# Kernel optimization log

Measured on AMD Instinct MI355X. Metric: run time of the kernel, lower is better.

The kernel has to match this reference:

```python
import jax, jax.numpy as jnp
import numpy as np

BS, N, D, B, D_PM = 8, 4096, 1024, 8, 64
BUDGET = 16.0


def setup_inputs() -> dict:
    key = jax.random.key(0)
    ks = jax.random.split(key, 6)
    H = jax.random.normal(ks[0], (BS, N, D), jnp.float32)
    surprise = jax.random.normal(ks[1], (BS, N, D), jnp.float32)
    # W_pm initialized as (1/B)*I + small noise, as in initialize()
    eye = jnp.eye(D_PM, dtype=jnp.float32)
    W_pm = eye / B + 0.01 * jax.random.normal(ks[2], (BS, B, D_PM, D_PM), jnp.float32)
    proj_in_w = jax.random.normal(ks[3], (D_PM, D), jnp.float32) / np.float32(np.sqrt(D))
    proj_in_b = jnp.zeros((D_PM,), jnp.float32)
    # original zero-inits proj_out; use small values so output is non-trivial
    proj_out_w = 0.02 * jax.random.normal(ks[4], (D, D_PM), jnp.float32)
    proj_out_b = jnp.zeros((D,), jnp.float32)
    raw_beta = jnp.full((B,), -3.0, jnp.float32)
    raw_decay = jnp.full((B,), np.float32(np.log(0.999 / 0.001)), jnp.float32)  # logit(0.999)
    surp_scale = jnp.ones((1,), jnp.float32)
    surp_bias = jnp.zeros((1,), jnp.float32)
    return dict(H=H, surprise=surprise, W_pm=W_pm,
                proj_in_w=proj_in_w, proj_in_b=proj_in_b,
                proj_out_w=proj_out_w, proj_out_b=proj_out_b,
                raw_beta=raw_beta, raw_decay=raw_decay,
                surp_scale=surp_scale, surp_bias=surp_bias)


def reference(H, surprise, W_pm, proj_in_w, proj_in_b, proj_out_w, proj_out_b,
              raw_beta, raw_decay, surp_scale, surp_bias):
    # ---- read ----
    pre = jnp.einsum('bnd,pd->bnp', H, proj_in_w) + proj_in_b          # [BS,N,D_pm]
    W_sum = jnp.sum(W_pm, axis=1)                                      # [BS,D_pm,D_pm]
    post = jnp.einsum('bnp,bqp->bnq', pre, W_sum)                      # pre @ W_sum^T
    pm_read = jnp.einsum('bnq,dq->bnd', post, proj_out_w) + proj_out_b # [BS,N,D]
    # ---- commit (Hebbian, surprise-gated) ----
    surp_mag = jnp.linalg.norm(surprise, axis=-1)                      # [BS,N]
    s = jax.nn.sigmoid(surp_scale * surp_mag + surp_bias)              # [BS,N]
    weighted = jnp.sqrt(s)[..., None] * pre                            # [BS,N,D_pm]
    G = jnp.einsum('bnp,bnq->bpq', weighted, weighted) / N             # [BS,D_pm,D_pm]
    beta = jax.nn.softplus(raw_beta)                                   # [B]
    decay = jax.nn.sigmoid(raw_decay)                                  # [B]
    eye = jnp.eye(D_PM, dtype=pre.dtype)
    T = decay[None, :, None, None] * eye + beta[None, :, None, None] * G[:, None]  # [BS,B,D_pm,D_pm]
    W_new = jnp.einsum('bkij,bkjq->bkiq', W_pm, T)                     # [BS,B,D_pm,D_pm]
    frob = jnp.sqrt(jnp.sum(W_new * W_new, axis=(-2, -1), keepdims=True))
    scale = jnp.minimum(BUDGET / jnp.maximum(frob, 1e-8), 1.0)
    W_new = W_new * scale
    return pm_read, W_new
```

## Files before the change

kernel.cpp:

```cpp
#include <hip/hip_runtime.h>

typedef unsigned short u16;
typedef __attribute__((ext_vector_type(4))) float f32x4;
typedef __attribute__((ext_vector_type(8))) short s16x8;

static constexpr int N_ = 4096;
static constexpr int D_ = 1024;

__device__ __forceinline__ u16 f2bf(float f) {
  unsigned u = __float_as_uint(f);
  u += 0x7FFFu + ((u >> 16) & 1u);
  return (u16)(u >> 16);
}

__device__ __forceinline__ f32x4 zero4() {
  f32x4 z; z[0] = 0.f; z[1] = 0.f; z[2] = 0.f; z[3] = 0.f; return z;
}

__global__ __launch_bounds__(256) void k_prep(
    const float* __restrict__ Wpm, const float* __restrict__ piw,
    const float* __restrict__ pw, u16* __restrict__ WpB,
    u16* __restrict__ MB) {
  int bid = blockIdx.x, tid = threadIdx.x;
  if (bid < 16) {
    size_t i0 = (size_t)bid * 4096;
    for (int idx = tid; idx < 4096; idx += 256)
      WpB[i0 + idx] = f2bf(piw[i0 + idx]);
    return;
  }
  __shared__ float Ws[64][65];
  int idx2 = bid - 16;
  int b = idx2 >> 4, t = idx2 & 15;
  for (int idx = tid; idx < 4096; idx += 256) {
    float s = 0.f;
#pragma unroll
    for (int k = 0; k < 8; ++k)
      s += Wpm[((size_t)(b * 8 + k)) * 4096 + idx];
    Ws[idx >> 6][idx & 63] = s;
  }
  __syncthreads();
  u16* mb = MB + ((size_t)b << 16);
  for (int oidx = tid; oidx < 4096; oidx += 256) {
    int r = oidx >> 6, c = oidx & 63;
    int drow = t * 64 + r;
    const float* prow = pw + (size_t)drow * 64;
    float acc = 0.f;
#pragma unroll 8
    for (int q = 0; q < 64; ++q) acc += prow[q] * Ws[q][c];
    mb[(size_t)drow * 64 + c] = f2bf(acc);
  }
}

__global__ __launch_bounds__(512, 4) void k_main(
    const float* __restrict__ H, const float* __restrict__ Sur,
    const float* __restrict__ pib, const float* __restrict__ pob,
    const float* __restrict__ sscale_p, const float* __restrict__ sbias_p,
    const u16* __restrict__ WpB, const u16* __restrict__ MB,
    float* __restrict__ Gacc, float* __restrict__ out) {
  __shared__ float preF[64][68];
  __shared__ u16 preRP[64][72];
  __shared__ u16 wRP[64][72];
  __shared__ float sqs[64];

  const int tid = threadIdx.x;
  const int lane = tid & 63;
  const int w = tid >> 6;
  const int wm = w & 3;
  const int wk = w >> 2;
  const int llo = lane & 15;
  const int lhi = lane >> 4;
  const int b = blockIdx.x >> 6;
  const int row0 = (blockIdx.x & 63) * 64;

  {
    int r = w * 8 + (lane >> 3);
    const float* p = Sur + ((size_t)b * N_ + row0 + r) * D_ + (lane & 7) * 4;
    float a0 = 0.f, a1 = 0.f;
#pragma unroll 8
    for (int j = 0; j < 32; j += 2) {
      float4 v = *(const float4*)(p + j * 32);
      float4 v2 = *(const float4*)(p + j * 32 + 32);
      a0 += v.x * v.x + v.y * v.y + v.z * v.z + v.w * v.w;
      a1 += v2.x * v2.x + v2.y * v2.y + v2.z * v2.z + v2.w * v2.w;
    }
    float a = a0 + a1;
    a += __shfl_xor(a, 1, 64);
    a += __shfl_xor(a, 2, 64);
    a += __shfl_xor(a, 4, 64);
    if ((lane & 7) == 0) {
      float mag = sqrtf(a);
      float s = 1.f / (1.f + __expf(-(sscale_p[0] * mag + sbias_p[0])));
      sqs[r] = sqrtf(s);
    }
  }

  f32x4 accA[4];
#pragma unroll
  for (int t = 0; t < 4; ++t) accA[t] = zero4();
  {
    const float* hrow =
        H + ((size_t)b * N_ + row0 + wm * 16 + llo) * D_ + wk * 512 + lhi * 8;
    const u16* wp0 = WpB + (size_t)llo * 1024 + wk * 512 + lhi * 8;
#pragma unroll 2
    for (int k0 = 0; k0 < 512; k0 += 32) {
      float4 a0 = *(const float4*)(hrow + k0);
      float4 a1 = *(const float4*)(hrow + k0 + 4);
      s16x8 af;
      af[0] = (short)f2bf(a0.x); af[1] = (short)f2bf(a0.y);
      af[2] = (short)f2bf(a0.z); af[3] = (short)f2bf(a0.w);
      af[4] = (short)f2bf(a1.x); af[5] = (short)f2bf(a1.y);
      af[6] = (short)f2bf(a1.z); af[7] = (short)f2bf(a1.w);
#pragma unroll
      for (int t = 0; t < 4; ++t) {
        s16x8 bf = *(const s16x8*)(wp0 + (size_t)t * 16 * 1024 + k0);
        accA[t] = __builtin_amdgcn_mfma_f32_16x16x32_bf16(af, bf, accA[t], 0, 0, 0);
      }
    }
  }
  if (wk == 1) {
#pragma unroll
    for (int t = 0; t < 4; ++t)
#pragma unroll
      for (int r = 0; r < 4; ++r)
        preF[wm * 16 + lhi * 4 + r][t * 16 + llo] = accA[t][r];
  }
  __syncthreads();
  if (wk == 0) {
#pragma unroll
    for (int t = 0; t < 4; ++t) {
      float bias = pib[t * 16 + llo];
#pragma unroll
      for (int r = 0; r < 4; ++r) {
        int row = wm * 16 + lhi * 4 + r;
        float v = accA[t][r] + preF[row][t * 16 + llo] + bias;
        preRP[row][t * 16 + llo] = f2bf(v);
        wRP[row][t * 16 + llo] = f2bf(v * sqs[row]);
      }
    }
  }
  __syncthreads();

  {
    f32x4 accG[4];
#pragma unroll
    for (int t = 0; t < 4; ++t) accG[t] = zero4();
    int kbase = wk * 32;
    s16x8 ag;
#pragma unroll
    for (int j = 0; j < 8; ++j)
      ag[j] = (short)wRP[kbase + lhi * 8 + j][wm * 16 + llo];
#pragma unroll
    for (int t = 0; t < 4; ++t) {
      s16x8 bg;
#pragma unroll
      for (int j = 0; j < 8; ++j)
        bg[j] = (short)wRP[kbase + lhi * 8 + j][t * 16 + llo];
      accG[t] = __builtin_amdgcn_mfma_f32_16x16x32_bf16(ag, bg, accG[t], 0, 0, 0);
    }
    float* gb = Gacc + (size_t)b * 4096;
#pragma unroll
    for (int t = 0; t < 4; ++t)
#pragma unroll
      for (int r = 0; r < 4; ++r)
        atomicAdd(gb + (wm * 16 + lhi * 4 + r) * 64 + t * 16 + llo, accG[t][r]);
  }

  {
    s16x8 ad0 = *(const s16x8*)&preRP[wm * 16 + llo][lhi * 8];
    s16x8 ad1 = *(const s16x8*)&preRP[wm * 16 + llo][32 + lhi * 8];
    const u16* mb = MB + ((size_t)b << 16);
    float* orow = out + ((size_t)b * N_ + row0 + wm * 16) * D_;
    int nend = wk * 512 + 512;
    for (int n0 = wk * 512; n0 < nend; n0 += 16) {
      s16x8 b0 = *(const s16x8*)(mb + (size_t)(n0 + llo) * 64 + lhi * 8);
      s16x8 b1 = *(const s16x8*)(mb + (size_t)(n0 + llo) * 64 + 32 + lhi * 8);
      f32x4 acc = zero4();
      acc = __builtin_amdgcn_mfma_f32_16x16x32_bf16(ad0, b0, acc, 0, 0, 0);
      acc = __builtin_amdgcn_mfma_f32_16x16x32_bf16(ad1, b1, acc, 0, 0, 0);
      float bias = pob[n0 + llo];
#pragma unroll
      for (int r = 0; r < 4; ++r)
        orow[(size_t)(lhi * 4 + r) * D_ + n0 + llo] = acc[r] + bias;
    }
  }
}

__global__ __launch_bounds__(256) void k_wnew(
    const float* __restrict__ Wpm, const float* __restrict__ Gacc,
    const float* __restrict__ rbeta, const float* __restrict__ rdecay,
    float* __restrict__ outW) {
  __shared__ float Wk[64][66];
  __shared__ float Gl[64][66];
  __shared__ float red[4];
  int bk = blockIdx.x;
  int b = bk >> 3, k = bk & 7;
  int tid = threadIdx.x;
  const float* wsrc = Wpm + (size_t)bk * 4096;
  const float* gsrc = Gacc + (size_t)b * 4096;
  for (int idx = tid; idx < 4096; idx += 256) {
    Wk[idx >> 6][idx & 63] = wsrc[idx];
    Gl[idx >> 6][idx & 63] = gsrc[idx];
  }
  __syncthreads();
  float beta = log1pf(__expf(rbeta[k]));
  float decay = 1.f / (1.f + __expf(-rdecay[k]));
  float bn = beta * (1.f / 4096.f);
  int q = tid & 63;
  int rbase = tid >> 6;
  float vals[16];
  float ss = 0.f;
#pragma unroll
  for (int i = 0; i < 16; ++i) {
    int row = i * 4 + rbase;
    float acc = 0.f;
#pragma unroll 8
    for (int j = 0; j < 64; ++j) acc += Wk[row][j] * Gl[j][q];
    float v = decay * Wk[row][q] + bn * acc;
    vals[i] = v;
    ss += v * v;
  }
#pragma unroll
  for (int m = 1; m < 64; m <<= 1) ss += __shfl_xor(ss, m, 64);
  if ((tid & 63) == 0) red[tid >> 6] = ss;
  __syncthreads();
  float frob = sqrtf(red[0] + red[1] + red[2] + red[3]);
  float scale = fminf(16.f / fmaxf(frob, 1e-8f), 1.f);
  float* dst = outW + (size_t)bk * 4096;
#pragma unroll
  for (int i = 0; i < 16; ++i) dst[i * 256 + tid] = vals[i] * scale;
}

extern "C" void kernel_launch(void* const* d_in, const int* in_sizes, int n_in,
                              void* d_out, int out_size, void* d_ws, size_t ws_size,
                              hipStream_t stream) {
  const float* H      = (const float*)d_in[0];
  const float* Sur    = (const float*)d_in[1];
  const float* Wpm    = (const float*)d_in[2];
  const float* piw    = (const float*)d_in[3];
  const float* pib    = (const float*)d_in[4];
  const float* pw     = (const float*)d_in[5];
  const float* pob    = (const float*)d_in[6];
  const float* rbeta  = (const float*)d_in[7];
  const float* rdecay = (const float*)d_in[8];
  const float* sscale = (const float*)d_in[9];
  const float* sbias  = (const float*)d_in[10];
  float* out = (float*)d_out;

  char* ws = (char*)d_ws;
  float* Gacc = (float*)(ws);
  u16* WpB    = (u16*)(ws + 131072);
  u16* MB     = (u16*)(ws + 262144);

  hipMemsetAsync(Gacc, 0, 131072, stream);
  k_prep<<<144, 256, 0, stream>>>(Wpm, piw, pw, WpB, MB);
  k_main<<<512, 512, 0, stream>>>(H, Sur, pib, pob, sscale, sbias,
                                  WpB, MB, Gacc, out);
  k_wnew<<<64, 256, 0, stream>>>(Wpm, Gacc, rbeta, rdecay,
                                 out + (size_t)8 * 4096 * 1024);
}
```

Before: 165.6 us.

## Pipeline H and MB loads via LDS, move surprise norms out, drop G atomics

```diff
diff --git a/kernel.cpp b/kernel.cpp
--- a/kernel.cpp
+++ b/kernel.cpp
@@ -1,11 +1,15 @@
 #include <hip/hip_runtime.h>
 
 typedef unsigned short u16;
+typedef unsigned int u32;
 typedef __attribute__((ext_vector_type(4))) float f32x4;
 typedef __attribute__((ext_vector_type(8))) short s16x8;
 
 static constexpr int N_ = 4096;
 static constexpr int D_ = 1024;
+
+#define WAITV(N) asm volatile("s_waitcnt vmcnt(" #N ")" ::: "memory")
+#define MEMCLOB() asm volatile("" ::: "memory")
 
 __device__ __forceinline__ u16 f2bf(float f) {
   unsigned u = __float_as_uint(f);
@@ -17,10 +21,18 @@
   f32x4 z; z[0] = 0.f; z[1] = 0.f; z[2] = 0.f; z[3] = 0.f; return z;
 }
 
-__global__ __launch_bounds__(256) void k_prep(
+__device__ __forceinline__ void gload16(const void* g, void* lds) {
+  __builtin_amdgcn_global_load_lds(
+      (const __attribute__((address_space(1))) u32*)g,
+      (__attribute__((address_space(3))) u32*)lds, 16, 0, 0);
+}
+
+__global__ __launch_bounds__(256) void k_aux(
     const float* __restrict__ Wpm, const float* __restrict__ piw,
-    const float* __restrict__ pw, u16* __restrict__ WpB,
-    u16* __restrict__ MB) {
+    const float* __restrict__ pw, const float* __restrict__ Sur,
+    const float* __restrict__ sscale_p, const float* __restrict__ sbias_p,
+    u16* __restrict__ WpB, u16* __restrict__ MB, float* __restrict__ sqs_ws) {
+  __shared__ float Ws[64][65];
   int bid = blockIdx.x, tid = threadIdx.x;
   if (bid < 16) {
     size_t i0 = (size_t)bid * 4096;
@@ -28,39 +40,71 @@
       WpB[i0 + idx] = f2bf(piw[i0 + idx]);
     return;
   }
-  __shared__ float Ws[64][65];
-  int idx2 = bid - 16;
-  int b = idx2 >> 4, t = idx2 & 15;
-  for (int idx = tid; idx < 4096; idx += 256) {
-    float s = 0.f;
-#pragma unroll
-    for (int k = 0; k < 8; ++k)
-      s += Wpm[((size_t)(b * 8 + k)) * 4096 + idx];
-    Ws[idx >> 6][idx & 63] = s;
-  }
-  __syncthreads();
-  u16* mb = MB + ((size_t)b << 16);
-  for (int oidx = tid; oidx < 4096; oidx += 256) {
-    int r = oidx >> 6, c = oidx & 63;
-    int drow = t * 64 + r;
-    const float* prow = pw + (size_t)drow * 64;
-    float acc = 0.f;
+  if (bid < 144) {
+    int idx2 = bid - 16;
+    int b = idx2 >> 4, t = idx2 & 15;
+    for (int idx = tid; idx < 4096; idx += 256) {
+      float s = 0.f;
+#pragma unroll
+      for (int k = 0; k < 8; ++k)
+        s += Wpm[((size_t)(b * 8 + k)) * 4096 + idx];
+      Ws[idx >> 6][idx & 63] = s;
+    }
+    __syncthreads();
+    u16* mb = MB + ((size_t)b << 16);
+    for (int oidx = tid; oidx < 4096; oidx += 256) {
+      int r = oidx >> 6, c = oidx & 63;
+      int drow = t * 64 + r;
+      const float* prow = pw + (size_t)drow * 64;
+      float acc = 0.f;
 #pragma unroll 8
-    for (int q = 0; q < 64; ++q) acc += prow[q] * Ws[q][c];
-    mb[(size_t)drow * 64 + c] = f2bf(acc);
+      for (int q = 0; q < 64; ++q) acc += prow[q] * Ws[q][c];
+      mb[(size_t)drow * 64 + c] = f2bf(acc);
+    }
+    return;
+  }
+  int w = tid >> 6, lane = tid & 63;
+  int fr = (bid - 144) * 16 + w * 4;
+  const float4* r0 = (const float4*)(Sur + (size_t)fr * 1024) + lane;
+  float s0 = 0.f, s1 = 0.f, s2 = 0.f, s3 = 0.f;
+#pragma unroll
+  for (int c = 0; c < 4; ++c) {
+    float4 v0 = r0[c * 64];
+    float4 v1 = r0[256 + c * 64];
+    float4 v2 = r0[512 + c * 64];
+    float4 v3 = r0[768 + c * 64];
+    s0 += v0.x * v0.x + v0.y * v0.y + v0.z * v0.z + v0.w * v0.w;
+    s1 += v1.x * v1.x + v1.y * v1.y + v1.z * v1.z + v1.w * v1.w;
+    s2 += v2.x * v2.x + v2.y * v2.y + v2.z * v2.z + v2.w * v2.w;
+    s3 += v3.x * v3.x + v3.y * v3.y + v3.z * v3.z + v3.w * v3.w;
+  }
+#pragma unroll
+  for (int m = 1; m < 64; m <<= 1) {
+    s0 += __shfl_xor(s0, m, 64);
+    s1 += __shfl_xor(s1, m, 64);
+    s2 += __shfl_xor(s2, m, 64);
+    s3 += __shfl_xor(s3, m, 64);
+  }
+  float res = s0;
+  if (lane == 1) res = s1;
+  if (lane == 2) res = s2;
+  if (lane == 3) res = s3;
+  if (lane < 4) {
+    float mag = sqrtf(res);
+    float s = 1.f / (1.f + __expf(-(sscale_p[0] * mag + sbias_p[0])));
+    sqs_ws[fr + lane] = sqrtf(s);
   }
 }
 
 __global__ __launch_bounds__(512, 4) void k_main(
-    const float* __restrict__ H, const float* __restrict__ Sur,
-    const float* __restrict__ pib, const float* __restrict__ pob,
-    const float* __restrict__ sscale_p, const float* __restrict__ sbias_p,
-    const u16* __restrict__ WpB, const u16* __restrict__ MB,
-    float* __restrict__ Gacc, float* __restrict__ out) {
-  __shared__ float preF[64][68];
-  __shared__ u16 preRP[64][72];
-  __shared__ u16 wRP[64][72];
-  __shared__ float sqs[64];
+    const float* __restrict__ H, const float* __restrict__ pib,
+    const float* __restrict__ pob, const u16* __restrict__ WpB,
+    const u16* __restrict__ MB, const float* __restrict__ sqs_ws,
+    float* __restrict__ Gpart, float* __restrict__ out) {
+  __shared__ __align__(16) char arena[32768];
+  __shared__ __align__(16) u16 preRP[64][72];
+  __shared__ __align__(16) u16 wRPT[64][72];
+  __shared__ float pobL[1024];
 
   const int tid = threadIdx.x;
   const int lane = tid & 63;
@@ -72,51 +116,74 @@
   const int b = blockIdx.x >> 6;
   const int row0 = (blockIdx.x & 63) * 64;
 
-  {
-    int r = w * 8 + (lane >> 3);
-    const float* p = Sur + ((size_t)b * N_ + row0 + r) * D_ + (lane & 7) * 4;
-    float a0 = 0.f, a1 = 0.f;
-#pragma unroll 8
-    for (int j = 0; j < 32; j += 2) {
-      float4 v = *(const float4*)(p + j * 32);
-      float4 v2 = *(const float4*)(p + j * 32 + 32);
-      a0 += v.x * v.x + v.y * v.y + v.z * v.z + v.w * v.w;
-      a1 += v2.x * v2.x + v2.y * v2.y + v2.z * v2.z + v2.w * v2.w;
-    }
-    float a = a0 + a1;
-    a += __shfl_xor(a, 1, 64);
-    a += __shfl_xor(a, 2, 64);
-    a += __shfl_xor(a, 4, 64);
-    if ((lane & 7) == 0) {
-      float mag = sqrtf(a);
-      float s = 1.f / (1.f + __expf(-(sscale_p[0] * mag + sbias_p[0])));
-      sqs[r] = sqrtf(s);
-    }
-  }
+  float bias_t[4];
+#pragma unroll
+  for (int t = 0; t < 4; ++t) bias_t[t] = pib[t * 16 + llo];
+  float sqs_r[4];
+#pragma unroll
+  for (int r = 0; r < 4; ++r)
+    sqs_r[r] = sqs_ws[b * 4096 + row0 + wm * 16 + lhi * 4 + r];
+
+  const int srow = 8 * w + (lane >> 3);
+  const int sc16 = (lane & 7) ^ (srow & 7);
 
   f32x4 accA[4];
 #pragma unroll
   for (int t = 0; t < 4; ++t) accA[t] = zero4();
-  {
-    const float* hrow =
-        H + ((size_t)b * N_ + row0 + wm * 16 + llo) * D_ + wk * 512 + lhi * 8;
-    const u16* wp0 = WpB + (size_t)llo * 1024 + wk * 512 + lhi * 8;
-#pragma unroll 2
-    for (int k0 = 0; k0 < 512; k0 += 32) {
-      float4 a0 = *(const float4*)(hrow + k0);
-      float4 a1 = *(const float4*)(hrow + k0 + 4);
-      s16x8 af;
-      af[0] = (short)f2bf(a0.x); af[1] = (short)f2bf(a0.y);
-      af[2] = (short)f2bf(a0.z); af[3] = (short)f2bf(a0.w);
-      af[4] = (short)f2bf(a1.x); af[5] = (short)f2bf(a1.y);
-      af[6] = (short)f2bf(a1.z); af[7] = (short)f2bf(a1.w);
-#pragma unroll
-      for (int t = 0; t < 4; ++t) {
-        s16x8 bf = *(const s16x8*)(wp0 + (size_t)t * 16 * 1024 + k0);
-        accA[t] = __builtin_amdgcn_mfma_f32_16x16x32_bf16(af, bf, accA[t], 0, 0, 0);
-      }
-    }
-  }
+
+  const float* hsrc = H + ((size_t)b * N_ + row0 + srow) * D_ + sc16 * 4;
+  const u16* wpb = WpB + (size_t)wk * 512 + lhi * 8;
+
+  s16x8 B0[4], B1[4];
+  auto LOADB = [&](int kc, s16x8* Bs) {
+#pragma unroll
+    for (int t = 0; t < 4; ++t)
+      Bs[t] = *(const s16x8*)(wpb + (size_t)(t * 16 + llo) * 1024 + kc * 32);
+  };
+  auto STAGEH = [&](int kc, int buf) {
+    gload16(hsrc + kc * 32, arena + buf * 16384 + w * 1024);
+    gload16(hsrc + 512 + kc * 32, arena + buf * 16384 + 8192 + w * 1024);
+  };
+  const int arow = wm * 16 + llo;
+  const int r7a = arow & 7;
+  auto COMPA = [&](int buf, const s16x8* Bs) {
+    const char* abase = arena + buf * 16384 + wk * 8192 + arow * 128;
+    f32x4 alo = *(const f32x4*)(abase + (((lhi * 2) ^ r7a) * 16));
+    f32x4 ahi = *(const f32x4*)(abase + (((lhi * 2 + 1) ^ r7a) * 16));
+    s16x8 af;
+    af[0] = (short)f2bf(alo[0]); af[1] = (short)f2bf(alo[1]);
+    af[2] = (short)f2bf(alo[2]); af[3] = (short)f2bf(alo[3]);
+    af[4] = (short)f2bf(ahi[0]); af[5] = (short)f2bf(ahi[1]);
+    af[6] = (short)f2bf(ahi[2]); af[7] = (short)f2bf(ahi[3]);
+#pragma unroll
+    for (int t = 0; t < 4; ++t)
+      accA[t] = __builtin_amdgcn_mfma_f32_16x16x32_bf16(af, Bs[t], accA[t], 0, 0, 0);
+  };
+
+  LOADB(0, B0); STAGEH(0, 0);
+  MEMCLOB();
+  LOADB(1, B1); STAGEH(1, 1);
+  MEMCLOB();
+
+  for (int kc = 0; kc < 16; kc += 2) {
+    WAITV(6);
+    __builtin_amdgcn_s_barrier();
+    COMPA(0, B0);
+    MEMCLOB();
+    __builtin_amdgcn_s_barrier();
+    if (kc + 2 < 16) { LOADB(kc + 2, B0); STAGEH(kc + 2, 0); }
+    MEMCLOB();
+    if (kc + 1 == 15) { WAITV(0); } else { WAITV(6); }
+    __builtin_amdgcn_s_barrier();
+    COMPA(1, B1);
+    MEMCLOB();
+    __builtin_amdgcn_s_barrier();
+    if (kc + 3 < 16) { LOADB(kc + 3, B1); STAGEH(kc + 3, 1); }
+    MEMCLOB();
+  }
+
+  __syncthreads();
+  float (*preF)[65] = (float(*)[65])arena;
   if (wk == 1) {
 #pragma unroll
     for (int t = 0; t < 4; ++t)
@@ -127,16 +194,14 @@
   __syncthreads();
   if (wk == 0) {
 #pragma unroll
-    for (int t = 0; t < 4; ++t) {
-      float bias = pib[t * 16 + llo];
+    for (int t = 0; t < 4; ++t)
 #pragma unroll
       for (int r = 0; r < 4; ++r) {
         int row = wm * 16 + lhi * 4 + r;
-        float v = accA[t][r] + preF[row][t * 16 + llo] + bias;
+        float v = accA[t][r] + preF[row][t * 16 + llo] + bias_t[t];
         preRP[row][t * 16 + llo] = f2bf(v);
-        wRP[row][t * 16 + llo] = f2bf(v * sqs[row]);
+        wRPT[t * 16 + llo][row] = f2bf(v * sqs_r[r]);
       }
-    }
   }
   __syncthreads();
 
@@ -144,63 +209,96 @@
     f32x4 accG[4];
 #pragma unroll
     for (int t = 0; t < 4; ++t) accG[t] = zero4();
-    int kbase = wk * 32;
-    s16x8 ag;
-#pragma unroll
-    for (int j = 0; j < 8; ++j)
-      ag[j] = (short)wRP[kbase + lhi * 8 + j][wm * 16 + llo];
+    s16x8 ag = *(const s16x8*)&wRPT[wm * 16 + llo][wk * 32 + lhi * 8];
 #pragma unroll
     for (int t = 0; t < 4; ++t) {
-      s16x8 bg;
-#pragma unroll
-      for (int j = 0; j < 8; ++j)
-        bg[j] = (short)wRP[kbase + lhi * 8 + j][t * 16 + llo];
+      s16x8 bg = *(const s16x8*)&wRPT[t * 16 + llo][wk * 32 + lhi * 8];
       accG[t] = __builtin_amdgcn_mfma_f32_16x16x32_bf16(ag, bg, accG[t], 0, 0, 0);
     }
-    float* gb = Gacc + (size_t)b * 4096;
+    float* gout = Gpart + ((size_t)blockIdx.x * 2 + wk) * 4096;
 #pragma unroll
     for (int t = 0; t < 4; ++t)
 #pragma unroll
       for (int r = 0; r < 4; ++r)
-        atomicAdd(gb + (wm * 16 + lhi * 4 + r) * 64 + t * 16 + llo, accG[t][r]);
-  }
-
-  {
-    s16x8 ad0 = *(const s16x8*)&preRP[wm * 16 + llo][lhi * 8];
-    s16x8 ad1 = *(const s16x8*)&preRP[wm * 16 + llo][32 + lhi * 8];
-    const u16* mb = MB + ((size_t)b << 16);
-    float* orow = out + ((size_t)b * N_ + row0 + wm * 16) * D_;
-    int nend = wk * 512 + 512;
-    for (int n0 = wk * 512; n0 < nend; n0 += 16) {
-      s16x8 b0 = *(const s16x8*)(mb + (size_t)(n0 + llo) * 64 + lhi * 8);
-      s16x8 b1 = *(const s16x8*)(mb + (size_t)(n0 + llo) * 64 + 32 + lhi * 8);
-      f32x4 acc = zero4();
-      acc = __builtin_amdgcn_mfma_f32_16x16x32_bf16(ad0, b0, acc, 0, 0, 0);
-      acc = __builtin_amdgcn_mfma_f32_16x16x32_bf16(ad1, b1, acc, 0, 0, 0);
-      float bias = pob[n0 + llo];
-#pragma unroll
-      for (int r = 0; r < 4; ++r)
-        orow[(size_t)(lhi * 4 + r) * D_ + n0 + llo] = acc[r] + bias;
-    }
+        gout[(wm * 16 + lhi * 4 + r) * 64 + t * 16 + llo] = accG[t][r];
+  }
+
+  pobL[tid] = pob[tid];
+  pobL[tid + 512] = pob[tid + 512];
+  __syncthreads();
+
+  const u16* mbb = MB + ((size_t)b << 16);
+  const u16* msrc0 = mbb + (size_t)srow * 64 + sc16 * 8;
+  auto STAGED = [&](int c, int buf) {
+    gload16(msrc0 + (size_t)c * 64 * 64, arena + buf * 16384 + w * 1024);
+    gload16(msrc0 + (size_t)(512 + c * 64) * 64, arena + buf * 16384 + 8192 + w * 1024);
+  };
+  s16x8 ad0 = *(const s16x8*)&preRP[wm * 16 + llo][lhi * 8];
+  s16x8 ad1 = *(const s16x8*)&preRP[wm * 16 + llo][32 + lhi * 8];
+  float* orow = out + ((size_t)b * N_ + row0 + wm * 16) * D_;
+
+  STAGED(0, 0);
+  MEMCLOB();
+  STAGED(1, 1);
+  MEMCLOB();
+  for (int c = 0; c < 8; ++c) {
+    if (c == 0) { WAITV(2); }
+    else if (c == 7) { WAITV(16); }
+    else { WAITV(18); }
+    __builtin_amdgcn_s_barrier();
+    {
+      const char* dbase = arena + (c & 1) * 16384 + wk * 8192;
+#pragma unroll
+      for (int i = 0; i < 4; ++i) {
+        int row = i * 16 + llo;
+        int r7 = row & 7;
+        const char* base = dbase + row * 128;
+        s16x8 b0 = *(const s16x8*)(base + ((lhi ^ r7) * 16));
+        s16x8 b1 = *(const s16x8*)(base + (((4 + lhi) ^ r7) * 16));
+        f32x4 acc = zero4();
+        acc = __builtin_amdgcn_mfma_f32_16x16x32_bf16(ad0, b0, acc, 0, 0, 0);
+        acc = __builtin_amdgcn_mfma_f32_16x16x32_bf16(ad1, b1, acc, 0, 0, 0);
+        int n0 = wk * 512 + c * 64 + i * 16;
+        float bias = pobL[n0 + llo];
+#pragma unroll
+        for (int r = 0; r < 4; ++r)
+          orow[(size_t)(lhi * 4 + r) * D_ + n0 + llo] = acc[r] + bias;
+      }
+    }
+    MEMCLOB();
+    __builtin_amdgcn_s_barrier();
+    if (c + 2 < 8) STAGED(c + 2, c & 1);
+    MEMCLOB();
   }
 }
 
 __global__ __launch_bounds__(256) void k_wnew(
-    const float* __restrict__ Wpm, const float* __restrict__ Gacc,
+    const float* __restrict__ Wpm, const float* __restrict__ Gpart,
     const float* __restrict__ rbeta, const float* __restrict__ rdecay,
     float* __restrict__ outW) {
-  __shared__ float Wk[64][66];
-  __shared__ float Gl[64][66];
+  __shared__ float Wk[64][68];
+  __shared__ float Gl[64][68];
   __shared__ float red[4];
   int bk = blockIdx.x;
   int b = bk >> 3, k = bk & 7;
   int tid = threadIdx.x;
+  f32x4 a0 = zero4(), a1 = zero4(), a2 = zero4(), a3 = zero4();
+  const float* gp = Gpart + (size_t)b * 128 * 4096 + tid * 16;
+#pragma unroll 2
+  for (int sl = 0; sl < 128; ++sl) {
+    const f32x4* p = (const f32x4*)(gp + (size_t)sl * 4096);
+    a0 += p[0]; a1 += p[1]; a2 += p[2]; a3 += p[3];
+  }
+  {
+    float* gl = &Gl[tid >> 2][(tid & 3) * 16];
+#pragma unroll
+    for (int j = 0; j < 4; ++j) {
+      gl[j] = a0[j]; gl[4 + j] = a1[j]; gl[8 + j] = a2[j]; gl[12 + j] = a3[j];
+    }
+  }
   const float* wsrc = Wpm + (size_t)bk * 4096;
-  const float* gsrc = Gacc + (size_t)b * 4096;
-  for (int idx = tid; idx < 4096; idx += 256) {
+  for (int idx = tid; idx < 4096; idx += 256)
     Wk[idx >> 6][idx & 63] = wsrc[idx];
-    Gl[idx >> 6][idx & 63] = gsrc[idx];
-  }
   __syncthreads();
   float beta = log1pf(__expf(rbeta[k]));
   float decay = 1.f / (1.f + __expf(-rdecay[k]));
@@ -247,14 +345,14 @@
   float* out = (float*)d_out;
 
   char* ws = (char*)d_ws;
-  float* Gacc = (float*)(ws);
-  u16* WpB    = (u16*)(ws + 131072);
-  u16* MB     = (u16*)(ws + 262144);
-
-  hipMemsetAsync(Gacc, 0, 131072, stream);
-  k_prep<<<144, 256, 0, stream>>>(Wpm, piw, pw, WpB, MB);
-  k_main<<<512, 512, 0, stream>>>(H, Sur, pib, pob, sscale, sbias,
-                                  WpB, MB, Gacc, out);
-  k_wnew<<<64, 256, 0, stream>>>(Wpm, Gacc, rbeta, rdecay,
+  u16* WpB      = (u16*)(ws);
+  u16* MB       = (u16*)(ws + 131072);
+  float* sqs_ws = (float*)(ws + 1179648);
+  float* Gpart  = (float*)(ws + 1310720);
+
+  k_aux<<<2192, 256, 0, stream>>>(Wpm, piw, pw, Sur, sscale, sbias,
+                                  WpB, MB, sqs_ws);
+  k_main<<<512, 512, 0, stream>>>(H, pib, pob, WpB, MB, sqs_ws, Gpart, out);
+  k_wnew<<<64, 256, 0, stream>>>(Wpm, Gpart, rbeta, rdecay,
                                  out + (size_t)8 * 4096 * 1024);
 }
```

Result: faster. 162.3 us (-2.0%).
